# Optimization experiments

Hardware: AMD Instinct MI355X
Metric: run time of the kernel (lower is better)

The kernel has to match this reference:

```python
import jax, jax.numpy as jnp
import numpy as np
import math

N = 131072   # number of points
C = 32       # embed_dim
K = 19       # num_class
ZD = 16      # z_dim
BN_EPS = 1e-4
SIG_THR = 0.8


def setup_inputs():
    key = jax.random.key(0)
    ks = jax.random.split(key, 16)
    f32 = jnp.float32
    rn = lambda k, s, sc=1.0: jax.random.normal(k, s, dtype=f32) * sc
    return {
        'feat': rn(ks[0], (N, C)),
        'scene_flow': rn(ks[1], (N, 3)),
        'coarse_pred': rn(ks[2], (N, K)),
        'z': rn(ks[3], (ZD,)),
        'select_w1': rn(ks[4], (C, C), 0.2),
        'bn_gamma': jnp.ones((C,), f32),
        'bn_beta': jnp.zeros((C,), f32),
        'bn_mean': jnp.zeros((C,), f32),
        'bn_var': jnp.ones((C,), f32),
        'select_w2': rn(ks[5], (C, 1), 0.2),
        'select_b2': jnp.zeros((1,), f32),
        'wq': rn(ks[6], (C, C), 0.2), 'bq': jnp.zeros((C,), f32),
        'wk': rn(ks[7], (C, C), 0.2), 'bk': jnp.zeros((C,), f32),
        'wv': rn(ks[8], (C, C), 0.2), 'bv': jnp.zeros((C,), f32),
        'wo': rn(ks[9], (C, C), 0.2), 'bo': jnp.zeros((C,), f32),
        'wt': rn(ks[10], (2 * C, C), 0.2), 'bt': jnp.zeros((C,), f32),
        'w_out': rn(ks[11], (C, K), 0.2), 'b_out': jnp.zeros((K,), f32),
        'w_gen': rn(ks[12], (ZD + K + 3, C), 0.2), 'b_gen': jnp.zeros((C,), f32),
    }


def _forward(feat, scene_flow, coarse_pred, z, select_w1, bn_gamma, bn_beta,
             bn_mean, bn_var, select_w2, select_b2, wq, bq, wk, bk, wv, bv,
             wo, bo, wt, bt, w_out, b_out, w_gen, b_gen):
    cp = jax.nn.softmax(coarse_pred, axis=-1)                      # (N, K)
    temp_mask = jnp.any(scene_flow != 0, axis=-1)                  # (N,)
    # select_mlp: Linear(no bias) -> BatchNorm(eval, eps=1e-4) -> ReLU -> Linear -> Sigmoid
    h = (feat @ select_w1 - bn_mean) / jnp.sqrt(bn_var + BN_EPS) * bn_gamma + bn_beta
    h = jnp.maximum(h, 0.0)
    score = jax.nn.sigmoid(h @ select_w2 + select_b2)[:, 0]        # (N,)
    valid = (score < SIG_THR) & temp_mask                          # (N,)
    # cvae stand-in: linear over concat(z, onehot(class), scene_flow) -> (N, K, C)
    wz, wc, ws = w_gen[:ZD], w_gen[ZD:ZD + K], w_gen[ZD + K:]
    gen = (z @ wz + b_gen)[None, None, :] + wc[None, :, :] + (scene_flow @ ws)[:, None, :]
    gen = gen * cp[:, :, None]                                     # scale by softmax prob
    # tiny cross-attention: 1 query per point over K=19 class prototypes
    q = feat @ wq + bq                                             # (N, C)
    k_ = jnp.einsum('nkc,cd->nkd', gen, wk) + bk                   # (N, K, C)
    v_ = jnp.einsum('nkc,cd->nkd', gen, wv) + bv                   # (N, K, C)
    attn = jax.nn.softmax(jnp.einsum('nd,nkd->nk', q, k_) / math.sqrt(C), axis=-1)
    aug = jnp.einsum('nk,nkd->nd', attn, v_) @ wo + bo             # (N, C)
    # scatter-back: invalid points get zeros (equivalent to torch boolean scatter)
    new_feat = jnp.where(valid[:, None], aug, 0.0)
    refine = jnp.concatenate([feat, new_feat], axis=-1) @ wt + bt  # (N, C)
    return refine @ w_out + b_out                                  # (N, K)


def reference(feat, scene_flow, coarse_pred, z, select_w1, bn_gamma, bn_beta,
              bn_mean, bn_var, select_w2, select_b2, wq, bq, wk, bk, wv, bv,
              wo, bo, wt, bt, w_out, b_out, w_gen, b_gen):
    return _forward(feat, scene_flow, coarse_pred, z, select_w1, bn_gamma,
                    bn_beta, bn_mean, bn_var, select_w2, select_b2, wq, bq,
                    wk, bk, wv, bv, wo, bo, wt, bt, w_out, b_out, w_gen, b_gen)
```

## Files before the change

kernel.cpp:

```cpp
#include <hip/hip_runtime.h>

#define NPTS 131072

constexpr int OFF_SW1 = 0;
constexpr int OFF_BNS = 1024;
constexpr int OFF_BNH = 1056;
constexpr int OFF_SW2 = 1088;
constexpr int OFF_B2  = 1120;
constexpr int TBL  = 1152;
constexpr int LQA  = 0;
constexpr int LGVB = 1280;
constexpr int LMVB = 1660;
constexpr int LQM  = 1720;
constexpr int LQGB = 1848;
constexpr int LBB  = 1868;
constexpr int LCV  = 1888;
constexpr int LQMB = 1908;
constexpr int XG   = 3328;
constexpr int XA2  = 3936;
constexpr int XMK  = 4544;
constexpr int XMV  = 4640;
constexpr int XGK  = 4736;
constexpr int XGV  = 5344;
constexpr int XB   = 5952;

#define CONST_AS __attribute__((address_space(4)))
__device__ __forceinline__ const CONST_AS float* to_const(const float* p) {
    return (const CONST_AS float*)p;
}

__global__ __launch_bounds__(256) void pre_a(
    const float* __restrict__ z,
    const float* __restrict__ sw1,
    const float* __restrict__ bn_gamma, const float* __restrict__ bn_beta,
    const float* __restrict__ bn_mean,  const float* __restrict__ bn_var,
    const float* __restrict__ sw2,      const float* __restrict__ sb2,
    const float* __restrict__ wk,
    const float* __restrict__ wv,
    const float* __restrict__ wt, const float* __restrict__ bt,
    const float* __restrict__ wout, const float* __restrict__ bout,
    const float* __restrict__ wgen, const float* __restrict__ bgen,
    float* __restrict__ W)
{
    int i = blockIdx.x * 256 + threadIdx.x;
    if (i < 1024) {
        W[OFF_SW1 + i] = sw1[(i & 31) * 32 + (i >> 5)];
    } else if (i < 1632) {
        int t = i - 1024, e = t / 19, j = t % 19;
        float a1 = 0.f, a2 = 0.f;
        for (int d = 0; d < 32; ++d) {
            float w_ = wout[d*19 + j];
            a1 += wt[e*32 + d] * w_;
            a2 += wt[(32 + e)*32 + d] * w_;
        }
        W[TBL + LQA + e*40 + 20 + j] = a1; W[XA2 + t] = a2;
    } else if (i < 2240) {
        int t = i - 1632, k = t >> 5, e = t & 31;
        float g = bgen[e];
        for (int d = 0; d < 16; ++d) g += z[d] * wgen[d*32 + e];
        W[XG + t] = g + wgen[(16 + k)*32 + e];
    } else if (i < 2336) {
        int t = i - 2240, m = t >> 5, c = t & 31;
        float a = 0.f, b = 0.f;
        for (int e = 0; e < 32; ++e) {
            float wsr = wgen[(35 + m)*32 + e];
            a += wsr * wk[e*32 + c];
            b += wsr * wv[e*32 + c];
        }
        W[XMK + t] = a; W[XMV + t] = b;
    } else if (i < 2368) {
        int t = i - 2336;
        float scale = bn_gamma[t] / sqrtf(bn_var[t] + 1e-4f);
        W[OFF_BNS + t] = scale;
        W[OFF_BNH + t] = bn_beta[t] - bn_mean[t] * scale;
        W[OFF_SW2 + t] = sw2[t];
    } else if (i < 2387) {
        int t = i - 2368;
        float a = bout[t];
        for (int d = 0; d < 32; ++d) a += bt[d] * wout[d*19 + t];
        W[TBL + LBB + t] = a;
    } else if (i == 2387) {
        W[OFF_B2] = sb2[0];
    } else if (i < 2452) {
        int t = i - 2388;
        if (t < 32)      W[TBL + LQA + t*40 + 19] = 0.f;
        else             W[TBL + LQA + (t-32)*40 + 39] = 0.f;
    }
}

__global__ __launch_bounds__(256) void pre_b(
    const float* __restrict__ wq, const float* __restrict__ bq,
    const float* __restrict__ wk, const float* __restrict__ wv,
    const float* __restrict__ wo,
    float* __restrict__ W)
{
    int i = blockIdx.x * 256 + threadIdx.x;
    if (i < 608) {
        int k = i >> 5, c = i & 31;
        float a = 0.f, b = 0.f;
        for (int e = 0; e < 32; ++e) {
            float g = W[XG + k*32 + e];
            a += g * wk[e*32 + c];
            b += g * wv[e*32 + c];
        }
        W[XGK + i] = a; W[XGV + i] = b;
    } else if (i < 1216) {
        int t = i - 608, c = t / 19, j = t % 19;
        float a = 0.f;
        for (int d = 0; d < 32; ++d) a += wo[c*32 + d] * W[XA2 + d*19 + j];
        W[XB + t] = a;
    } else if (i < 1312) {
        int t = i - 1216, e = t / 3, m = t % 3;
        float a = 0.f;
        for (int c = 0; c < 32; ++c) a += wq[e*32 + c] * W[XMK + m*32 + c];
        W[TBL + LQM + e*4 + m] = a;
    } else if (i < 1315) {
        int m = i - 1312;
        float a = 0.f;
        for (int c = 0; c < 32; ++c) a += bq[c] * W[XMK + m*32 + c];
        W[TBL + LQMB + m] = a;
    } else if (i < 1347) {
        int e = i - 1315;
        W[TBL + LQM + e*4 + 3] = 0.f;
    } else if (i == 1347) {
        W[TBL + LQMB + 3] = 0.f;
    }
}

__global__ __launch_bounds__(256) void pre_c(
    const float* __restrict__ wq, const float* __restrict__ bq,
    const float* __restrict__ bv, const float* __restrict__ bo,
    float* __restrict__ W)
{
    int i = blockIdx.x * 256 + threadIdx.x;
    if (i < 608) {
        int e = i / 19, k = i % 19;
        float a = 0.f;
        for (int c = 0; c < 32; ++c) a += wq[e*32 + c] * W[XGK + k*32 + c];
        W[TBL + LQA + e*40 + k] = a;
    } else if (i < 627) {
        int k = i - 608;
        float a = 0.f;
        for (int c = 0; c < 32; ++c) a += bq[c] * W[XGK + k*32 + c];
        W[TBL + LQGB + k] = a;
    } else if (i < 988) {
        int t = i - 627, k = t / 19, j = t % 19;
        float a = 0.f;
        for (int c = 0; c < 32; ++c) a += W[XGV + k*32 + c] * W[XB + c*19 + j];
        W[TBL + LGVB + k*20 + j] = a;
    } else if (i < 1045) {
        int t = i - 988, m = t / 19, j = t % 19;
        float a = 0.f;
        for (int c = 0; c < 32; ++c) a += W[XMV + m*32 + c] * W[XB + c*19 + j];
        W[TBL + LMVB + m*20 + j] = a;
    } else if (i < 1064) {
        int j = i - 1045;
        float a = 0.f;
        for (int c = 0; c < 32; ++c) a += bv[c] * W[XB + c*19 + j];
        for (int d = 0; d < 32; ++d) a += bo[d] * W[XA2 + d*19 + j];
        W[TBL + LCV + j] = a;
    } else if (i < 1108) {
        int t = i - 1064;
        if (t < 19)      W[TBL + LGVB + t*20 + 19] = 0.f;
        else if (t < 22) W[TBL + LMVB + (t-19)*20 + 19] = 0.f;
        else if (t == 22) W[TBL + LQGB + 19] = 0.f;
        else if (t == 23) W[TBL + LBB + 19] = 0.f;
        else if (t == 24) W[TBL + LCV + 19] = 0.f;
    }
}

__global__ __launch_bounds__(256, 2) void main_k(
    const float* __restrict__ feat,
    const float* __restrict__ sflow,
    const float* __restrict__ cpred,
    const float* __restrict__ Wg,
    float* __restrict__ out)
{
    const CONST_AS float* W = to_const(Wg);
    const int t = threadIdx.x;
    const int n = blockIdx.x * 256 + t;

    __shared__ __align__(16) float T[1912];
    __shared__ float F[32 * 256];

    {
        const float4* src = (const float4*)(Wg + TBL);
        float4* dst = (float4*)T;
        dst[t] = src[t];
        if (t < 222) dst[256 + t] = src[256 + t];
    }

    float f[32];
    {
        const float4* fp = (const float4*)(feat + (long)n * 32);
#pragma unroll
        for (int g = 0; g < 8; ++g) {
            float4 v = fp[g];
            f[g*4+0] = v.x; f[g*4+1] = v.y; f[g*4+2] = v.z; f[g*4+3] = v.w;
        }
    }
#pragma unroll
    for (int e = 0; e < 32; ++e) F[e*256 + t] = f[e];
    __syncthreads();

    float s0 = sflow[(long)n*3 + 0];
    float s1 = sflow[(long)n*3 + 1];
    float s2 = sflow[(long)n*3 + 2];
    bool tmask = (s0 != 0.f) | (s1 != 0.f) | (s2 != 0.f);

    float cp[19];
#pragma unroll
    for (int k = 0; k < 19; ++k) cp[k] = cpred[(long)n*19 + k];
    float m1 = cp[0];
#pragma unroll
    for (int k = 1; k < 19; ++k) m1 = fmaxf(m1, cp[k]);
    float sum1 = 0.f;
#pragma unroll
    for (int k = 0; k < 19; ++k) { cp[k] = __expf(cp[k] - m1); sum1 += cp[k]; }
    float r1 = 1.f / sum1;
#pragma unroll
    for (int k = 0; k < 19; ++k) cp[k] *= r1;

    float sacc = W[OFF_B2];
#pragma unroll 2
    for (int c = 0; c < 32; ++c) {
        float a = 0.f;
#pragma unroll
        for (int e = 0; e < 32; ++e) a = fmaf(f[e], W[OFF_SW1 + c*32 + e], a);
        float h = fmaxf(fmaf(a, W[OFF_BNS + c], W[OFF_BNH + c]), 0.f);
        sacc = fmaf(h, W[OFF_SW2 + c], sacc);
    }
    bool valid = tmask && (sacc < 1.3862943611198906f);

    float qg[19], o[19];
#pragma unroll
    for (int k = 0; k < 19; ++k) { qg[k] = T[LQGB + k]; o[k] = T[LBB + k]; }
    float qm0 = T[LQMB + 0], qm1 = T[LQMB + 1], qm2 = T[LQMB + 2];
#pragma unroll 4
    for (int e = 0; e < 32; ++e) {
        float fe = F[e*256 + t];
#pragma unroll
        for (int k = 0; k < 19; ++k) qg[k] = fmaf(fe, T[LQA + e*40 + k], qg[k]);
#pragma unroll
        for (int k = 0; k < 19; ++k) o[k]  = fmaf(fe, T[LQA + e*40 + 20 + k], o[k]);
        qm0 = fmaf(fe, T[LQM + e*4 + 0], qm0);
        qm1 = fmaf(fe, T[LQM + e*4 + 1], qm1);
        qm2 = fmaf(fe, T[LQM + e*4 + 2], qm2);
    }
    float qs = s0*qm0 + s1*qm1 + s2*qm2;

    const float RS = 0.17677669529663687f;
    float l[19];
#pragma unroll
    for (int k = 0; k < 19; ++k) l[k] = (cp[k] * (qg[k] + qs)) * RS;

    float m2 = l[0];
#pragma unroll
    for (int k = 1; k < 19; ++k) m2 = fmaxf(m2, l[k]);
    float sum2 = 0.f;
#pragma unroll
    for (int k = 0; k < 19; ++k) { l[k] = __expf(l[k] - m2); sum2 += l[k]; }
    float r2 = 1.f / sum2;
    float Sw = 0.f;
#pragma unroll
    for (int k = 0; k < 19; ++k) { l[k] = l[k] * r2 * cp[k]; Sw += l[k]; }

    float a2[19];
#pragma unroll
    for (int j = 0; j < 19; ++j) a2[j] = T[LCV + j];
    float c0 = Sw * s0, c1 = Sw * s1, c2 = Sw * s2;
#pragma unroll
    for (int j = 0; j < 19; ++j) a2[j] = fmaf(c0, T[LMVB + j], a2[j]);
#pragma unroll
    for (int j = 0; j < 19; ++j) a2[j] = fmaf(c1, T[LMVB + 20 + j], a2[j]);
#pragma unroll
    for (int j = 0; j < 19; ++j) a2[j] = fmaf(c2, T[LMVB + 40 + j], a2[j]);
#pragma unroll
    for (int k = 0; k < 19; ++k) {
        float lk = l[k];
#pragma unroll
        for (int j = 0; j < 19; ++j) a2[j] = fmaf(lk, T[LGVB + k*20 + j], a2[j]);
    }

    float vg = valid ? 1.f : 0.f;
    float* op = out + (long)n * 19;
#pragma unroll
    for (int j = 0; j < 19; ++j) op[j] = fmaf(vg, a2[j], o[j]);
}

extern "C" void kernel_launch(void* const* d_in, const int* in_sizes, int n_in,
                              void* d_out, int out_size, void* d_ws, size_t ws_size,
                              hipStream_t stream) {
    const float* feat  = (const float*)d_in[0];
    const float* sflow = (const float*)d_in[1];
    const float* cpred = (const float*)d_in[2];
    const float* z     = (const float*)d_in[3];
    const float* sw1   = (const float*)d_in[4];
    const float* bn_g  = (const float*)d_in[5];
    const float* bn_b  = (const float*)d_in[6];
    const float* bn_m  = (const float*)d_in[7];
    const float* bn_v  = (const float*)d_in[8];
    const float* sw2   = (const float*)d_in[9];
    const float* sb2   = (const float*)d_in[10];
    const float* wq    = (const float*)d_in[11];
    const float* bq    = (const float*)d_in[12];
    const float* wk    = (const float*)d_in[13];
    const float* bk    = (const float*)d_in[14];  (void)bk;
    const float* wv    = (const float*)d_in[15];
    const float* bv    = (const float*)d_in[16];
    const float* wo    = (const float*)d_in[17];
    const float* bo    = (const float*)d_in[18];
    const float* wt    = (const float*)d_in[19];
    const float* bt    = (const float*)d_in[20];
    const float* wout  = (const float*)d_in[21];
    const float* bout  = (const float*)d_in[22];
    const float* wgen  = (const float*)d_in[23];
    const float* bgen  = (const float*)d_in[24];

    float* W = (float*)d_ws;

    hipLaunchKernelGGL(pre_a, dim3(10), dim3(256), 0, stream,
                       z, sw1, bn_g, bn_b, bn_m, bn_v, sw2, sb2,
                       wk, wv, wt, bt, wout, bout, wgen, bgen, W);
    hipLaunchKernelGGL(pre_b, dim3(6), dim3(256), 0, stream,
                       wq, bq, wk, wv, wo, W);
    hipLaunchKernelGGL(pre_c, dim3(5), dim3(256), 0, stream,
                       wq, bq, bv, bo, W);

    hipLaunchKernelGGL(main_k, dim3(512), dim3(256), 0, stream,
                       feat, sflow, cpred, W, (float*)d_out);
}
```

Measured before the change: 150.9 us.

## Move per-point feature projections onto bf16 MFMA with split-precision select path

Replaces the scalar FMA loops that project each point's 32-dim feature through the select MLP weights and the fused query/output tables with bf16 MFMA 16x16x32 instructions. A new pre-kernel packs the weights into MFMA fragment layout. The select-MLP hidden layer uses a hi/lo bf16 split for near-fp32 accuracy, and points whose score lands near the threshold are recomputed in full fp32 under a wave ballot. The other projections are kept in bf16 in shared memory, which lowers the precision of the attention logits and output, and it adds an extra preprocessing launch plus more shared memory per block.

```diff
diff --git a/kernel.cpp b/kernel.cpp
--- a/kernel.cpp
+++ b/kernel.cpp
@@ -1,32 +1,36 @@
 #include <hip/hip_runtime.h>
 
 #define NPTS 131072
+
+typedef __attribute__((ext_vector_type(8))) short short8;
+typedef __attribute__((ext_vector_type(4))) float f32x4;
 
 constexpr int OFF_SW1 = 0;
 constexpr int OFF_BNS = 1024;
 constexpr int OFF_BNH = 1056;
 constexpr int OFF_SW2 = 1088;
 constexpr int OFF_B2  = 1120;
-constexpr int TBL  = 1152;
-constexpr int LQA  = 0;
-constexpr int LGVB = 1280;
-constexpr int LMVB = 1660;
-constexpr int LQM  = 1720;
-constexpr int LQGB = 1848;
-constexpr int LBB  = 1868;
-constexpr int LCV  = 1888;
-constexpr int LQMB = 1908;
-constexpr int XG   = 3328;
-constexpr int XA2  = 3936;
-constexpr int XMK  = 4544;
-constexpr int XMV  = 4640;
-constexpr int XGK  = 4736;
-constexpr int XGV  = 5344;
-constexpr int XB   = 5952;
+constexpr int OFF_QGB = 1121;
+constexpr int OFF_QMB = 1140;
+constexpr int OFF_BB  = 1143;
+constexpr int OFF_CV  = 1162;
+constexpr int OFF_MVB = 1181;
+constexpr int EGVB    = 1240;
+constexpr int FRAGH   = 1620;
+constexpr int FRAGL   = 2900;
+constexpr int XA1 = 3412, XA2 = 4020, XG = 4628, XMK = 5236, XMV = 5332;
+constexpr int XGK = 5428, XGV = 6036, XB = 6644, XQG = 7252, XQM = 7860;
 
 #define CONST_AS __attribute__((address_space(4)))
 __device__ __forceinline__ const CONST_AS float* to_const(const float* p) {
     return (const CONST_AS float*)p;
+}
+__device__ __forceinline__ unsigned b16r(float x) {
+    unsigned u = __float_as_uint(x);
+    return (u + 0x7fffu + ((u >> 16) & 1u)) >> 16;
+}
+__device__ __forceinline__ float fromb(unsigned h) {
+    return __uint_as_float(h << 16);
 }
 
 __global__ __launch_bounds__(256) void pre_a(
@@ -35,8 +39,7 @@
     const float* __restrict__ bn_gamma, const float* __restrict__ bn_beta,
     const float* __restrict__ bn_mean,  const float* __restrict__ bn_var,
     const float* __restrict__ sw2,      const float* __restrict__ sb2,
-    const float* __restrict__ wk,
-    const float* __restrict__ wv,
+    const float* __restrict__ wk, const float* __restrict__ wv,
     const float* __restrict__ wt, const float* __restrict__ bt,
     const float* __restrict__ wout, const float* __restrict__ bout,
     const float* __restrict__ wgen, const float* __restrict__ bgen,
@@ -53,7 +56,7 @@
             a1 += wt[e*32 + d] * w_;
             a2 += wt[(32 + e)*32 + d] * w_;
         }
-        W[TBL + LQA + e*40 + 20 + j] = a1; W[XA2 + t] = a2;
+        W[XA1 + t] = a1; W[XA2 + t] = a2;
     } else if (i < 2240) {
         int t = i - 1632, k = t >> 5, e = t & 31;
         float g = bgen[e];
@@ -78,13 +81,9 @@
         int t = i - 2368;
         float a = bout[t];
         for (int d = 0; d < 32; ++d) a += bt[d] * wout[d*19 + t];
-        W[TBL + LBB + t] = a;
+        W[OFF_BB + t] = a;
     } else if (i == 2387) {
         W[OFF_B2] = sb2[0];
-    } else if (i < 2452) {
-        int t = i - 2388;
-        if (t < 32)      W[TBL + LQA + t*40 + 19] = 0.f;
-        else             W[TBL + LQA + (t-32)*40 + 39] = 0.f;
     }
 }
 
@@ -113,17 +112,12 @@
         int t = i - 1216, e = t / 3, m = t % 3;
         float a = 0.f;
         for (int c = 0; c < 32; ++c) a += wq[e*32 + c] * W[XMK + m*32 + c];
-        W[TBL + LQM + e*4 + m] = a;
+        W[XQM + t] = a;
     } else if (i < 1315) {
         int m = i - 1312;
         float a = 0.f;
         for (int c = 0; c < 32; ++c) a += bq[c] * W[XMK + m*32 + c];
-        W[TBL + LQMB + m] = a;
-    } else if (i < 1347) {
-        int e = i - 1315;
-        W[TBL + LQM + e*4 + 3] = 0.f;
-    } else if (i == 1347) {
-        W[TBL + LQMB + 3] = 0.f;
+        W[OFF_QMB + m] = a;
     }
 }
 
@@ -137,35 +131,57 @@
         int e = i / 19, k = i % 19;
         float a = 0.f;
         for (int c = 0; c < 32; ++c) a += wq[e*32 + c] * W[XGK + k*32 + c];
-        W[TBL + LQA + e*40 + k] = a;
+        W[XQG + i] = a;
     } else if (i < 627) {
         int k = i - 608;
         float a = 0.f;
         for (int c = 0; c < 32; ++c) a += bq[c] * W[XGK + k*32 + c];
-        W[TBL + LQGB + k] = a;
+        W[OFF_QGB + k] = a;
     } else if (i < 988) {
         int t = i - 627, k = t / 19, j = t % 19;
         float a = 0.f;
         for (int c = 0; c < 32; ++c) a += W[XGV + k*32 + c] * W[XB + c*19 + j];
-        W[TBL + LGVB + k*20 + j] = a;
-    } else if (i < 1045) {
-        int t = i - 988, m = t / 19, j = t % 19;
+        W[EGVB + k*20 + j] = a;
+    } else if (i < 1007) {
+        int k = i - 988;
+        W[EGVB + k*20 + 19] = 0.f;
+    } else if (i < 1064) {
+        int t = i - 1007, m = t / 19, j = t % 19;
         float a = 0.f;
         for (int c = 0; c < 32; ++c) a += W[XMV + m*32 + c] * W[XB + c*19 + j];
-        W[TBL + LMVB + m*20 + j] = a;
-    } else if (i < 1064) {
-        int j = i - 1045;
+        W[OFF_MVB + t] = a;
+    } else if (i < 1083) {
+        int j = i - 1064;
         float a = 0.f;
         for (int c = 0; c < 32; ++c) a += bv[c] * W[XB + c*19 + j];
         for (int d = 0; d < 32; ++d) a += bo[d] * W[XA2 + d*19 + j];
-        W[TBL + LCV + j] = a;
-    } else if (i < 1108) {
-        int t = i - 1064;
-        if (t < 19)      W[TBL + LGVB + t*20 + 19] = 0.f;
-        else if (t < 22) W[TBL + LMVB + (t-19)*20 + 19] = 0.f;
-        else if (t == 22) W[TBL + LQGB + 19] = 0.f;
-        else if (t == 23) W[TBL + LBB + 19] = 0.f;
-        else if (t == 24) W[TBL + LCV + 19] = 0.f;
+        W[OFF_CV + j] = a;
+    }
+}
+
+__global__ __launch_bounds__(256) void pre_d(
+    const float* __restrict__ sw1, float* __restrict__ W)
+{
+    int i = blockIdx.x * 256 + threadIdx.x;
+    unsigned short* FH = (unsigned short*)(W + FRAGH);
+    unsigned short* FL = (unsigned short*)(W + FRAGL);
+    if (i < 2560) {
+        int T = i >> 9, l = (i >> 3) & 63, j = i & 7;
+        int e = ((l >> 4) << 3) + j, col = 16*T + (l & 15);
+        float v;
+        if      (col < 32) v = sw1[e*32 + col];
+        else if (col < 51) v = W[XQG + e*19 + (col - 32)];
+        else if (col < 70) v = W[XA1 + e*19 + (col - 51)];
+        else if (col < 73) v = W[XQM + e*3  + (col - 70)];
+        else               v = 0.f;
+        FH[(T*64 + l)*8 + j] = (unsigned short)b16r(v);
+    } else if (i < 3584) {
+        int i2 = i - 2560;
+        int T = i2 >> 9, l = (i2 >> 3) & 63, j = i2 & 7;
+        int e = ((l >> 4) << 3) + j, col = 16*T + (l & 15);
+        float v = sw1[e*32 + col];
+        float vh = fromb(b16r(v));
+        FL[(T*64 + l)*8 + j] = (unsigned short)b16r(v - vh);
     }
 }
 
@@ -177,40 +193,81 @@
     float* __restrict__ out)
 {
     const CONST_AS float* W = to_const(Wg);
-    const int t = threadIdx.x;
-    const int n = blockIdx.x * 256 + t;
-
-    __shared__ __align__(16) float T[1912];
-    __shared__ float F[32 * 256];
-
-    {
-        const float4* src = (const float4*)(Wg + TBL);
-        float4* dst = (float4*)T;
-        dst[t] = src[t];
-        if (t < 222) dst[256 + t] = src[256 + t];
-    }
-
-    float f[32];
-    {
-        const float4* fp = (const float4*)(feat + (long)n * 32);
-#pragma unroll
-        for (int g = 0; g < 8; ++g) {
-            float4 v = fp[g];
-            f[g*4+0] = v.x; f[g*4+1] = v.y; f[g*4+2] = v.z; f[g*4+3] = v.w;
-        }
-    }
-#pragma unroll
-    for (int e = 0; e < 32; ++e) F[e*256 + t] = f[e];
+    const int t = threadIdx.x, lane = t & 63, wvi = t >> 6;
+    const int pblk = blockIdx.x * 256;
+
+    __shared__ __align__(16) float HF[32 * 264];
+    __shared__ __align__(16) unsigned short OH[41 * 264];
+    __shared__ __align__(16) float GV[380];
+
+    if (t < 95) ((float4*)GV)[t] = ((const float4*)(Wg + EGVB))[t];
+
+    const short8* FH8 = (const short8*)(Wg + FRAGH);
+    const short8* FL8 = (const short8*)(Wg + FRAGL);
+    short8 bh0 = FH8[0*64 + lane], bh1 = FH8[1*64 + lane];
+    short8 bh2 = FH8[2*64 + lane], bh3 = FH8[3*64 + lane];
+    short8 bh4 = FH8[4*64 + lane];
+    short8 bl0 = FL8[0*64 + lane], bl1 = FL8[1*64 + lane];
+
+    const int n15 = lane & 15, q = lane >> 4;
+
+#pragma unroll
+    for (int tile = 0; tile < 4; ++tile) {
+        const int p0 = wvi*64 + tile*16;
+        const float* fr = feat + (long)(pblk + p0 + n15) * 32 + q*8;
+        float xv[8];
+        {
+            float4 va = *(const float4*)fr;
+            float4 vb = *(const float4*)(fr + 4);
+            xv[0]=va.x; xv[1]=va.y; xv[2]=va.z; xv[3]=va.w;
+            xv[4]=vb.x; xv[5]=vb.y; xv[6]=vb.z; xv[7]=vb.w;
+        }
+        short8 ah, al;
+#pragma unroll
+        for (int j = 0; j < 8; ++j) {
+            unsigned h = b16r(xv[j]);
+            ah[j] = (short)h;
+            al[j] = (short)b16r(xv[j] - fromb(h));
+        }
+        f32x4 z4 = {0.f, 0.f, 0.f, 0.f};
+        f32x4 aH0, aH1, a2_, a3_, a4_;
+        aH0 = __builtin_amdgcn_mfma_f32_16x16x32_bf16(ah, bh0, z4, 0, 0, 0);
+        aH0 = __builtin_amdgcn_mfma_f32_16x16x32_bf16(ah, bl0, aH0, 0, 0, 0);
+        aH0 = __builtin_amdgcn_mfma_f32_16x16x32_bf16(al, bh0, aH0, 0, 0, 0);
+        aH1 = __builtin_amdgcn_mfma_f32_16x16x32_bf16(ah, bh1, z4, 0, 0, 0);
+        aH1 = __builtin_amdgcn_mfma_f32_16x16x32_bf16(ah, bl1, aH1, 0, 0, 0);
+        aH1 = __builtin_amdgcn_mfma_f32_16x16x32_bf16(al, bh1, aH1, 0, 0, 0);
+        a2_ = __builtin_amdgcn_mfma_f32_16x16x32_bf16(ah, bh2, z4, 0, 0, 0);
+        a3_ = __builtin_amdgcn_mfma_f32_16x16x32_bf16(ah, bh3, z4, 0, 0, 0);
+        a4_ = __builtin_amdgcn_mfma_f32_16x16x32_bf16(ah, bh4, z4, 0, 0, 0);
+
+        *(f32x4*)&HF[(n15)      * 264 + p0 + q*4] = aH0;
+        *(f32x4*)&HF[(16 + n15) * 264 + p0 + q*4] = aH1;
+        {
+            unsigned d0, d1;
+            d0 = b16r(a2_[0]) | (b16r(a2_[1]) << 16);
+            d1 = b16r(a2_[2]) | (b16r(a2_[3]) << 16);
+            *(uint2*)&OH[(n15) * 264 + p0 + q*4] = make_uint2(d0, d1);
+            d0 = b16r(a3_[0]) | (b16r(a3_[1]) << 16);
+            d1 = b16r(a3_[2]) | (b16r(a3_[3]) << 16);
+            *(uint2*)&OH[(16 + n15) * 264 + p0 + q*4] = make_uint2(d0, d1);
+            if (n15 <= 8) {
+                d0 = b16r(a4_[0]) | (b16r(a4_[1]) << 16);
+                d1 = b16r(a4_[2]) | (b16r(a4_[3]) << 16);
+                *(uint2*)&OH[(32 + n15) * 264 + p0 + q*4] = make_uint2(d0, d1);
+            }
+        }
+    }
     __syncthreads();
 
-    float s0 = sflow[(long)n*3 + 0];
-    float s1 = sflow[(long)n*3 + 1];
-    float s2 = sflow[(long)n*3 + 2];
+    const long p = pblk + t;
+
+    float s0 = sflow[p*3 + 0], s1 = sflow[p*3 + 1], s2 = sflow[p*3 + 2];
     bool tmask = (s0 != 0.f) | (s1 != 0.f) | (s2 != 0.f);
 
     float cp[19];
 #pragma unroll
-    for (int k = 0; k < 19; ++k) cp[k] = cpred[(long)n*19 + k];
+    for (int k = 0; k < 19; ++k) cp[k] = cpred[p*19 + k];
     float m1 = cp[0];
 #pragma unroll
     for (int k = 1; k < 19; ++k) m1 = fmaxf(m1, cp[k]);
@@ -221,38 +278,45 @@
 #pragma unroll
     for (int k = 0; k < 19; ++k) cp[k] *= r1;
 
+    const float TH = 1.3862943611198906f;
     float sacc = W[OFF_B2];
-#pragma unroll 2
+#pragma unroll
     for (int c = 0; c < 32; ++c) {
-        float a = 0.f;
-#pragma unroll
-        for (int e = 0; e < 32; ++e) a = fmaf(f[e], W[OFF_SW1 + c*32 + e], a);
+        float a = HF[c*264 + t];
         float h = fmaxf(fmaf(a, W[OFF_BNS + c], W[OFF_BNH + c]), 0.f);
         sacc = fmaf(h, W[OFF_SW2 + c], sacc);
     }
-    bool valid = tmask && (sacc < 1.3862943611198906f);
-
-    float qg[19], o[19];
-#pragma unroll
-    for (int k = 0; k < 19; ++k) { qg[k] = T[LQGB + k]; o[k] = T[LBB + k]; }
-    float qm0 = T[LQMB + 0], qm1 = T[LQMB + 1], qm2 = T[LQMB + 2];
-#pragma unroll 4
-    for (int e = 0; e < 32; ++e) {
-        float fe = F[e*256 + t];
-#pragma unroll
-        for (int k = 0; k < 19; ++k) qg[k] = fmaf(fe, T[LQA + e*40 + k], qg[k]);
-#pragma unroll
-        for (int k = 0; k < 19; ++k) o[k]  = fmaf(fe, T[LQA + e*40 + 20 + k], o[k]);
-        qm0 = fmaf(fe, T[LQM + e*4 + 0], qm0);
-        qm1 = fmaf(fe, T[LQM + e*4 + 1], qm1);
-        qm2 = fmaf(fe, T[LQM + e*4 + 2], qm2);
-    }
+    bool nearthr = fabsf(sacc - TH) < 1e-3f;
+    if (__ballot(nearthr) != 0ULL) {
+        float f[32];
+        const float4* fp4 = (const float4*)(feat + p*32);
+#pragma unroll
+        for (int g = 0; g < 8; ++g) {
+            float4 v = fp4[g];
+            f[g*4+0]=v.x; f[g*4+1]=v.y; f[g*4+2]=v.z; f[g*4+3]=v.w;
+        }
+        float sr = W[OFF_B2];
+        for (int c = 0; c < 32; ++c) {
+            float a = 0.f;
+#pragma unroll
+            for (int e = 0; e < 32; ++e) a = fmaf(f[e], W[OFF_SW1 + c*32 + e], a);
+            float h = fmaxf(fmaf(a, W[OFF_BNS + c], W[OFF_BNH + c]), 0.f);
+            sr = fmaf(h, W[OFF_SW2 + c], sr);
+        }
+        sacc = nearthr ? sr : sacc;
+    }
+    bool valid = tmask && (sacc < TH);
+
+    float qm0 = fromb(OH[38*264 + t]) + W[OFF_QMB + 0];
+    float qm1 = fromb(OH[39*264 + t]) + W[OFF_QMB + 1];
+    float qm2 = fromb(OH[40*264 + t]) + W[OFF_QMB + 2];
     float qs = s0*qm0 + s1*qm1 + s2*qm2;
 
     const float RS = 0.17677669529663687f;
     float l[19];
 #pragma unroll
-    for (int k = 0; k < 19; ++k) l[k] = (cp[k] * (qg[k] + qs)) * RS;
+    for (int k = 0; k < 19; ++k)
+        l[k] = (cp[k] * (fromb(OH[k*264 + t]) + W[OFF_QGB + k] + qs)) * RS;
 
     float m2 = l[0];
 #pragma unroll
@@ -265,25 +329,25 @@
 #pragma unroll
     for (int k = 0; k < 19; ++k) { l[k] = l[k] * r2 * cp[k]; Sw += l[k]; }
 
+    float o[19];
+#pragma unroll
+    for (int j = 0; j < 19; ++j) o[j] = fromb(OH[(19 + j)*264 + t]) + W[OFF_BB + j];
+
     float a2[19];
-#pragma unroll
-    for (int j = 0; j < 19; ++j) a2[j] = T[LCV + j];
     float c0 = Sw * s0, c1 = Sw * s1, c2 = Sw * s2;
 #pragma unroll
-    for (int j = 0; j < 19; ++j) a2[j] = fmaf(c0, T[LMVB + j], a2[j]);
-#pragma unroll
-    for (int j = 0; j < 19; ++j) a2[j] = fmaf(c1, T[LMVB + 20 + j], a2[j]);
-#pragma unroll
-    for (int j = 0; j < 19; ++j) a2[j] = fmaf(c2, T[LMVB + 40 + j], a2[j]);
+    for (int j = 0; j < 19; ++j)
+        a2[j] = W[OFF_CV + j] + c0 * W[OFF_MVB + j]
+              + c1 * W[OFF_MVB + 19 + j] + c2 * W[OFF_MVB + 38 + j];
 #pragma unroll
     for (int k = 0; k < 19; ++k) {
         float lk = l[k];
 #pragma unroll
-        for (int j = 0; j < 19; ++j) a2[j] = fmaf(lk, T[LGVB + k*20 + j], a2[j]);
+        for (int j = 0; j < 19; ++j) a2[j] = fmaf(lk, GV[k*20 + j], a2[j]);
     }
 
     float vg = valid ? 1.f : 0.f;
-    float* op = out + (long)n * 19;
+    float* op = out + p * 19;
 #pragma unroll
     for (int j = 0; j < 19; ++j) op[j] = fmaf(vg, a2[j], o[j]);
 }
@@ -326,6 +390,8 @@
                        wq, bq, wk, wv, wo, W);
     hipLaunchKernelGGL(pre_c, dim3(5), dim3(256), 0, stream,
                        wq, bq, bv, bo, W);
+    hipLaunchKernelGGL(pre_d, dim3(14), dim3(256), 0, stream,
+                       sw1, W);
 
     hipLaunchKernelGGL(main_k, dim3(512), dim3(256), 0, stream,
                        feat, sflow, cpred, W, (float*)d_out);
```

New measurement: 141.7 us. 6.1% less time.
